# Kernel tuning notes

Measured on AMD Instinct MI355X. Metric: run time of the kernel, lower is better.

The kernel has to match this reference:

```python
import jax, jax.numpy as jnp
import numpy as np

B, L, DIM = 1, 2048, 4096
H, KV, HD = 32, 8, 128
REP = H // KV
SCALE = HD ** -0.5
ROPE_BASE = 10000.0


def rope_traditional(x, offset=0):
    # x: [B, H, L, D] ; traditional RoPE rotates interleaved pairs (x[2i], x[2i+1])
    D = x.shape[-1]
    Lx = x.shape[2]
    pos = jnp.arange(offset, offset + Lx, dtype=jnp.float32)            # [L]
    inv_freq = ROPE_BASE ** (-jnp.arange(0, D, 2, dtype=jnp.float32) / D)  # [D/2]
    ang = pos[:, None] * inv_freq[None, :]                               # [L, D/2]
    c, s = jnp.cos(ang), jnp.sin(ang)
    x1 = x[..., 0::2]
    x2 = x[..., 1::2]
    r1 = x1 * c - x2 * s
    r2 = x1 * s + x2 * c
    return jnp.stack([r1, r2], axis=-1).reshape(x.shape).astype(x.dtype)


def setup_inputs() -> dict:
    key = jax.random.key(0)
    k0, k1, k2, k3, k4 = jax.random.split(key, 5)
    x = jax.random.normal(k0, (B, L, DIM), dtype=jnp.float32)
    wq = jax.random.normal(k1, (DIM, H * HD), dtype=jnp.float32) * 0.02
    wk = jax.random.normal(k2, (DIM, KV * HD), dtype=jnp.float32) * 0.02
    wv = jax.random.normal(k3, (DIM, KV * HD), dtype=jnp.float32) * 0.02
    wo = jax.random.normal(k4, (H * HD, DIM), dtype=jnp.float32) * 0.02
    # additive causal mask (prefill)
    causal = jnp.tril(jnp.ones((L, L), dtype=bool))
    mask = jnp.where(causal, 0.0, -1e9).astype(jnp.float32)
    return {"x": x, "wq": wq, "wk": wk, "wv": wv, "wo": wo, "mask": mask}


def reference(x, wq, wk, wv, wo, mask):
    Bx, Lx, _ = x.shape
    q = (x @ wq).reshape(Bx, Lx, H, HD).transpose(0, 2, 1, 3)   # [B,H,L,hd]
    k = (x @ wk).reshape(Bx, Lx, KV, HD).transpose(0, 2, 1, 3)  # [B,KV,L,hd]
    v = (x @ wv).reshape(Bx, Lx, KV, HD).transpose(0, 2, 1, 3)
    # GQA head repeat (each kv head repeated REP times contiguously)
    k = jnp.repeat(k, REP, axis=1)  # [B,H,L,hd]
    v = jnp.repeat(v, REP, axis=1)
    # RoPE applied after repeat (cache=None branch), offset 0
    q = rope_traditional(q)
    k = rope_traditional(k)
    scores = jnp.einsum("bhld,bhmd->bhlm", q * SCALE, k) + mask  # [B,H,L,L]
    probs = jax.nn.softmax(scores.astype(jnp.float32), axis=-1).astype(scores.dtype)
    out = jnp.einsum("bhlm,bhmd->bhld", probs, v)
    out = out.transpose(0, 2, 1, 3).reshape(Bx, Lx, H * HD)
    return out @ wo, k, v
```

## Files before the change

kernel.cpp:

```cpp
#include <hip/hip_runtime.h>
#include <hip/hip_bf16.h>
#include <math.h>


#define L_SEQ 2048
#define DIM   4096
#define NH    32
#define NKV   8
#define HD    128
#define SCALE 0.08838834764831845f

typedef __bf16 bf16x8 __attribute__((ext_vector_type(8)));
typedef __bf16 bf16x4 __attribute__((ext_vector_type(4)));
typedef __bf16 bf16x2 __attribute__((ext_vector_type(2)));
typedef float  f32x4  __attribute__((ext_vector_type(4)));

__device__ __forceinline__ void gld16(const void* g, void* l) {
  __builtin_amdgcn_global_load_lds(
      (const __attribute__((address_space(1))) void*)g,
      (__attribute__((address_space(3))) void*)l, 16, 0, 0);
}

__global__ void cast_bf16_kernel(const float* __restrict__ in,
                                 __bf16* __restrict__ out, long n4) {
  long i = blockIdx.x * (long)blockDim.x + threadIdx.x;
  if (i >= n4) return;
  float4 f = reinterpret_cast<const float4*>(in)[i];
  bf16x4 o;
  o[0] = (__bf16)f.x; o[1] = (__bf16)f.y; o[2] = (__bf16)f.z; o[3] = (__bf16)f.w;
  reinterpret_cast<bf16x4*>(out)[i] = o;
}

__global__ void tcast_kernel(const float* __restrict__ in0, __bf16* __restrict__ out0,
                             const float* __restrict__ in1, __bf16* __restrict__ out1,
                             int K, int N) {
  __shared__ float tile[32][33];
  const float* in  = blockIdx.z ? in1  : in0;
  __bf16*     out  = blockIdx.z ? out1 : out0;
  int n0 = blockIdx.x * 32, k0 = blockIdx.y * 32;
  int tx = threadIdx.x & 31, ty = threadIdx.x >> 5;
#pragma unroll
  for (int i = 0; i < 4; ++i)
    tile[ty + i * 8][tx] = in[(long)(k0 + ty + i * 8) * N + n0 + tx];
  __syncthreads();
#pragma unroll
  for (int i = 0; i < 4; ++i)
    out[(long)(n0 + ty + i * 8) * K + k0 + tx] = (__bf16)tile[tx][ty + i * 8];
}

__global__ __launch_bounds__(256) void gemm128(
    const __bf16* __restrict__ A, const __bf16* __restrict__ B0,
    const __bf16* __restrict__ B1, void* __restrict__ C0, void* __restrict__ C1,
    int M, int N, int K, int mode) {
  __shared__ __bf16 As[128 * 64] __attribute__((aligned(16)));
  __shared__ __bf16 Bs[128 * 64] __attribute__((aligned(16)));
  const __bf16* Bt = blockIdx.z ? B1 : B0;
  void* C = blockIdx.z ? C1 : C0;
  const int m0 = blockIdx.y * 128, n0 = blockIdx.x * 128;
  const int t = threadIdx.x, wave = t >> 6, lane = t & 63;
  const int quad = lane >> 4, l16 = lane & 15;
  const int wm = (wave >> 1) * 64, wn = (wave & 1) * 64;

  int ar[4], ak[4];
#pragma unroll
  for (int it = 0; it < 4; ++it) {
    int c = it * 256 + t;
    ar[it] = c >> 3;
    ak[it] = ((c & 7) ^ (ar[it] & 7)) * 8;
  }

  f32x4 acc[4][4] = {};

  for (int kt = 0; kt < K; kt += 64) {
    __syncthreads();
#pragma unroll
    for (int it = 0; it < 4; ++it) {
      gld16(A  + (long)(m0 + ar[it]) * K + kt + ak[it],
            (char*)As + (size_t)(it * 256 + wave * 64) * 16);
      gld16(Bt + (long)(n0 + ar[it]) * K + kt + ak[it],
            (char*)Bs + (size_t)(it * 256 + wave * 64) * 16);
    }
    __syncthreads();
#pragma unroll
    for (int ks = 0; ks < 2; ++ks) {
      bf16x8 af[4], bfr[4];
      const int sw = ((ks * 4 + quad) ^ (l16 & 7)) * 16;
#pragma unroll
      for (int i = 0; i < 4; ++i) {
        af[i]  = *(const bf16x8*)((char*)As + (wm + i * 16 + l16) * 128 + sw);
        bfr[i] = *(const bf16x8*)((char*)Bs + (wn + i * 16 + l16) * 128 + sw);
      }
#pragma unroll
      for (int tm = 0; tm < 4; ++tm)
#pragma unroll
        for (int tn = 0; tn < 4; ++tn)
          acc[tm][tn] = __builtin_amdgcn_mfma_f32_16x16x32_bf16(
              af[tm], bfr[tn], acc[tm][tn], 0, 0, 0);
    }
  }
#pragma unroll
  for (int tm = 0; tm < 4; ++tm)
#pragma unroll
    for (int tn = 0; tn < 4; ++tn)
#pragma unroll
      for (int r = 0; r < 4; ++r) {
        int row = m0 + wm + tm * 16 + quad * 4 + r;
        int col = n0 + wn + tn * 16 + l16;
        float v = acc[tm][tn][r];
        if (mode == 0) {
          ((float*)C)[(long)row * N + col] = v;
        } else {
          long idx = ((long)(col >> 7) * L_SEQ + row) * HD + (col & 127);
          ((__bf16*)C)[idx] = (__bf16)v;
        }
      }
}

#define NLOG2_10K 13.287712379549449f

__global__ void rope_q_kernel(__bf16* __restrict__ q ) {
  int idx = blockIdx.x * blockDim.x + threadIdx.x;
  int i = idx & 63, l = (idx >> 6) & 2047, h = idx >> 17;
  if (h >= NH) return;
  long base = ((long)h * L_SEQ + l) * HD + 2 * i;
  bf16x2 x12 = *(bf16x2*)(q + base);
  float x1 = (float)x12[0], x2 = (float)x12[1];
  float inv = exp2f((float)i * (-NLOG2_10K / 64.0f));
  float s, c; __sincosf((float)l * inv, &s, &c);
  bf16x2 o; o[0] = (__bf16)(x1 * c - x2 * s); o[1] = (__bf16)(x1 * s + x2 * c);
  *(bf16x2*)(q + base) = o;
}

__global__ void ropekv_kernel(__bf16* __restrict__ kb ,
                              const __bf16* __restrict__ vb,
                              float* __restrict__ kout ,
                              float* __restrict__ vout) {
  int idx = blockIdx.x * blockDim.x + threadIdx.x;
  int i = idx & 63, l = (idx >> 6) & 2047, kv = idx >> 17;
  if (kv >= NKV) return;
  long base = ((long)kv * L_SEQ + l) * HD + 2 * i;
  bf16x2 x12 = *(bf16x2*)(kb + base);
  float x1 = (float)x12[0], x2 = (float)x12[1];
  float inv = exp2f((float)i * (-NLOG2_10K / 64.0f));
  float s, c; __sincosf((float)l * inv, &s, &c);
  float r1 = x1 * c - x2 * s, r2 = x1 * s + x2 * c;
  bf16x2 o; o[0] = (__bf16)r1; o[1] = (__bf16)r2;
  *(bf16x2*)(kb + base) = o;
  float2 kf; kf.x = r1; kf.y = r2;
  bf16x2 vv = *(const bf16x2*)(vb + base);
  float2 vf; vf.x = (float)vv[0]; vf.y = (float)vv[1];
  long off = (long)(kv * 4) * L_SEQ * HD + (long)l * HD + 2 * i;
#pragma unroll
  for (int rr = 0; rr < 4; ++rr) {
    *(float2*)(kout + off) = kf;
    *(float2*)(vout + off) = vf;
    off += (long)L_SEQ * HD;
  }
}

__global__ void vtrans_kernel(const __bf16* __restrict__ Vh, __bf16* __restrict__ Vt) {
  __shared__ __bf16 tile[64 * 65];
  int kv = blockIdx.z, lb = blockIdx.x * 64, db = blockIdx.y * 64;
  int t = threadIdx.x;
#pragma unroll
  for (int it = 0; it < 2; ++it) {
    int c = it * 256 + t, r = c >> 3, pc = c & 7;
    bf16x8 v = *(const bf16x8*)(Vh + ((long)kv * L_SEQ + lb + r) * HD + db + pc * 8);
#pragma unroll
    for (int e = 0; e < 8; ++e) tile[r * 65 + pc * 8 + e] = v[e];
  }
  __syncthreads();
#pragma unroll
  for (int it = 0; it < 2; ++it) {
    int c = it * 256 + t, r = c >> 3, pc = c & 7;
    bf16x8 v;
#pragma unroll
    for (int e = 0; e < 8; ++e) v[e] = tile[(pc * 8 + e) * 65 + r];
    *(bf16x8*)(Vt + ((long)kv * HD + db + r) * L_SEQ + lb + pc * 8) = v;
  }
}

#define PSP 72

__global__ __launch_bounds__(256) void attn3_kernel(
    const __bf16* __restrict__ Q, const __bf16* __restrict__ K,
    const __bf16* __restrict__ Vt, __bf16* __restrict__ O ) {
  __shared__ __bf16 Ks[2][64 * 128]  __attribute__((aligned(16)));
  __shared__ __bf16 Vts[2][128 * 64] __attribute__((aligned(16)));
  __shared__ __bf16 Ps[64 * PSP]     __attribute__((aligned(16)));

  const int p = blockIdx.x;
  const int h = blockIdx.y;
  const int t = threadIdx.x, wave = t >> 6, lane = t & 63;
  const int quad = lane >> 4, l16 = lane & 15;
  const int mw = wave * 16;
  const __bf16* Kh = K  + (long)(h >> 2) * L_SEQ * HD;
  const __bf16* Vh = Vt + (long)(h >> 2) * HD * L_SEQ;
  const float SL2 = SCALE * 1.44269504f;

  int kr[4], kk[4], vr[4], vk[4];
#pragma unroll
  for (int it = 0; it < 4; ++it) {
    int c = it * 256 + t;
    kr[it] = c >> 4; kk[it] = ((c & 15) ^ (kr[it] & 7)) * 8;
    vr[it] = c >> 3; vk[it] = ((c & 7)  ^ (vr[it] & 7)) * 8;
  }

#pragma unroll 1
  for (int tsel = 0; tsel < 2; ++tsel) {
    const int qb = tsel ? (31 - p) : p;
    const int l0 = qb * 64;
    const int mq = l0 + mw + l16;

    bf16x8 bq[4];
    {
      const __bf16* qrow = Q + ((long)h * L_SEQ + mq) * HD + quad * 8;
#pragma unroll
      for (int d = 0; d < 4; ++d) bq[d] = *(const bf16x8*)(qrow + d * 32);
    }

    f32x4 o_acc[8] = {};
    float m_run = -1e30f, l_run = 0.f;

    __syncthreads();
#pragma unroll
    for (int it = 0; it < 4; ++it) {
      gld16(Kh + (long)(0 + kr[it]) * HD + kk[it],
            (char*)Ks[0] + (size_t)(it * 256 + wave * 64) * 16);
      gld16(Vh + (long)vr[it] * L_SEQ + 0 + vk[it],
            (char*)Vts[0] + (size_t)(it * 256 + wave * 64) * 16);
    }

#pragma unroll 1
    for (int j = 0; j <= qb; ++j) {
      const int cur = j & 1;
      __syncthreads();
      if (j < qb) {
        const int nxt = cur ^ 1;
#pragma unroll
        for (int it = 0; it < 4; ++it) {
          gld16(Kh + (long)((j + 1) * 64 + kr[it]) * HD + kk[it],
                (char*)Ks[nxt] + (size_t)(it * 256 + wave * 64) * 16);
          gld16(Vh + (long)vr[it] * L_SEQ + (j + 1) * 64 + vk[it],
                (char*)Vts[nxt] + (size_t)(it * 256 + wave * 64) * 16);
        }
      }

      f32x4 s[4] = {};
#pragma unroll
      for (int dsi = 0; dsi < 4; ++dsi)
#pragma unroll
        for (int tn = 0; tn < 4; ++tn) {
          bf16x8 ak = *(const bf16x8*)((char*)Ks[cur] + (tn * 16 + l16) * 256 +
                                       (((dsi * 4 + quad) ^ (l16 & 7)) * 16));
          s[tn] = __builtin_amdgcn_mfma_f32_16x16x32_bf16(ak, bq[dsi], s[tn], 0, 0, 0);
        }

#pragma unroll
      for (int tn = 0; tn < 4; ++tn)
#pragma unroll
        for (int r = 0; r < 4; ++r) {
          float v = s[tn][r] * SL2;
          if (j == qb && (j * 64 + tn * 16 + quad * 4 + r) > mq) v = -3.0e38f;
          s[tn][r] = v;
        }
      float mx = -3.0e38f;
#pragma unroll
      for (int tn = 0; tn < 4; ++tn)
#pragma unroll
        for (int r = 0; r < 4; ++r) mx = fmaxf(mx, s[tn][r]);
      mx = fmaxf(mx, __shfl_xor(mx, 16, 64));
      mx = fmaxf(mx, __shfl_xor(mx, 32, 64));
      float mnew = fmaxf(m_run, mx);
      float alpha = exp2f(m_run - mnew);
      float rs = 0.f;
#pragma unroll
      for (int tn = 0; tn < 4; ++tn)
#pragma unroll
        for (int r = 0; r < 4; ++r) {
          float pe = exp2f(s[tn][r] - mnew);
          s[tn][r] = pe; rs += pe;
        }
      rs += __shfl_xor(rs, 16, 64);
      rs += __shfl_xor(rs, 32, 64);
      l_run = l_run * alpha + rs;
      m_run = mnew;

#pragma unroll
      for (int tn = 0; tn < 4; ++tn) {
        bf16x4 pv;
#pragma unroll
        for (int r = 0; r < 4; ++r) pv[r] = (__bf16)s[tn][r];
        *(bf16x4*)(&Ps[(mw + l16) * PSP + tn * 16 + quad * 4]) = pv;
      }

#pragma unroll
      for (int td = 0; td < 8; ++td)
#pragma unroll
        for (int r = 0; r < 4; ++r) o_acc[td][r] *= alpha;
#pragma unroll
      for (int ks = 0; ks < 2; ++ks) {
        bf16x8 bp = *(const bf16x8*)(&Ps[(mw + l16) * PSP + ks * 32 + quad * 8]);
#pragma unroll
        for (int td = 0; td < 8; ++td) {
          bf16x8 av = *(const bf16x8*)((char*)Vts[cur] + (td * 16 + l16) * 128 +
                                       (((ks * 4 + quad) ^ (l16 & 7)) * 16));
          o_acc[td] = __builtin_amdgcn_mfma_f32_16x16x32_bf16(av, bp, o_acc[td], 0, 0, 0);
        }
      }
    }

    float inv_l = 1.0f / l_run;
#pragma unroll
    for (int td = 0; td < 8; ++td) {
      bf16x4 ov;
#pragma unroll
      for (int r = 0; r < 4; ++r) ov[r] = (__bf16)(o_acc[td][r] * inv_l);
      *(bf16x4*)(O + (long)mq * DIM + h * HD + td * 16 + quad * 4) = ov;
    }
  }
}

extern "C" void kernel_launch(void* const* d_in, const int* in_sizes, int n_in,
                              void* d_out, int out_size, void* d_ws, size_t ws_size,
                              hipStream_t stream) {
  const float* x  = (const float*)d_in[0];
  const float* wq = (const float*)d_in[1];
  const float* wk = (const float*)d_in[2];
  const float* wv = (const float*)d_in[3];
  const float* wo = (const float*)d_in[4];

  float* out   = (float*)d_out;
  float* k_out = out + (long)L_SEQ * DIM;
  float* v_out = k_out + (long)NH * L_SEQ * HD;

  char* ws = (char*)d_ws;
  __bf16* Xb  = (__bf16*)ws; ws += (long)L_SEQ * DIM * 2;
  __bf16* Wqt = (__bf16*)ws; ws += (long)DIM * DIM * 2;
  __bf16* Wkt = (__bf16*)ws; ws += (long)DIM * (NKV * HD) * 2;
  __bf16* Wvt = (__bf16*)ws; ws += (long)DIM * (NKV * HD) * 2;
  __bf16* Wot = (__bf16*)ws; ws += (long)DIM * DIM * 2;
  __bf16* Qh  = (__bf16*)ws; ws += (long)NH * L_SEQ * HD * 2;
  __bf16* Kh  = (__bf16*)ws; ws += (long)NKV * L_SEQ * HD * 2;
  __bf16* Vh  = (__bf16*)ws; ws += (long)NKV * L_SEQ * HD * 2;
  __bf16* Vt  = (__bf16*)ws; ws += (long)NKV * HD * L_SEQ * 2;
  __bf16* Ob  = (__bf16*)ws; ws += (long)L_SEQ * DIM * 2;

  tcast_kernel<<<dim3(DIM / 32, DIM / 32, 1), 256, 0, stream>>>(wq, Wqt, wq, Wqt, DIM, DIM);
  tcast_kernel<<<dim3((NKV * HD) / 32, DIM / 32, 2), 256, 0, stream>>>(wk, Wkt, wv, Wvt, DIM, NKV * HD);
  tcast_kernel<<<dim3(DIM / 32, DIM / 32, 1), 256, 0, stream>>>(wo, Wot, wo, Wot, DIM, DIM);
  {
    long n = (long)L_SEQ * DIM;
    cast_bf16_kernel<<<dim3(n / 1024), 256, 0, stream>>>(x, Xb, n / 4);
  }
  gemm128<<<dim3(DIM / 128, L_SEQ / 128, 1), 256, 0, stream>>>(
      Xb, Wqt, Wqt, Qh, Qh, L_SEQ, DIM, DIM, 2);
  gemm128<<<dim3((NKV * HD) / 128, L_SEQ / 128, 2), 256, 0, stream>>>(
      Xb, Wkt, Wvt, Kh, Vh, L_SEQ, NKV * HD, DIM, 2);
  rope_q_kernel<<<dim3((NH * L_SEQ * 64) / 256), 256, 0, stream>>>(Qh);
  ropekv_kernel<<<dim3((NKV * L_SEQ * 64) / 256), 256, 0, stream>>>(Kh, Vh, k_out, v_out);
  vtrans_kernel<<<dim3(L_SEQ / 64, HD / 64, NKV), 256, 0, stream>>>(Vh, Vt);
  attn3_kernel<<<dim3(16, NH), 256, 0, stream>>>(Qh, Kh, Vt, Ob);
  gemm128<<<dim3(DIM / 128, L_SEQ / 128, 1), 256, 0, stream>>>(
      Ob, Wot, Wot, out, out, L_SEQ, DIM, DIM, 0);
}
```

Before: 615.1 us.

## Replace 128x128 GEMM with triple-buffered 128x256 pipelined GEMM and block swizzle

The projection GEMM moves from 128x128 tiles on 256 threads to 128x256 tiles on 512 threads. It uses a three-stage LDS ring filled by async global-to-LDS loads, and `s_waitcnt vmcnt` lets the next tile's loads overlap the current tile's MFMAs instead of forcing a full sync every K step. A workgroup index swizzle is meant to improve L2 reuse, and `s_setprio` raises priority around the MFMA bursts. The cost is about 144KB of LDS per block, so occupancy is limited to one block per CU, and the KV projection now launches fewer workgroups.

```diff
diff --git a/kernel.cpp b/kernel.cpp
--- a/kernel.cpp
+++ b/kernel.cpp
@@ -48,56 +48,136 @@
     out[(long)(n0 + ty + i * 8) * K + k0 + tx] = (__bf16)tile[tx][ty + i * 8];
 }
 
-__global__ __launch_bounds__(256) void gemm128(
+#define GBM 128
+#define GBN 256
+#define ABYTES  (GBM * 64 * 2)
+#define BBYTES  (GBN * 64 * 2)
+#define BUFBYTES (ABYTES + BBYTES)
+
+__global__ __launch_bounds__(512, 2) void gemm256(
     const __bf16* __restrict__ A, const __bf16* __restrict__ B0,
     const __bf16* __restrict__ B1, void* __restrict__ C0, void* __restrict__ C1,
     int M, int N, int K, int mode) {
-  __shared__ __bf16 As[128 * 64] __attribute__((aligned(16)));
-  __shared__ __bf16 Bs[128 * 64] __attribute__((aligned(16)));
+  __shared__ char lds[3 * BUFBYTES] __attribute__((aligned(16)));
   const __bf16* Bt = blockIdx.z ? B1 : B0;
   void* C = blockIdx.z ? C1 : C0;
-  const int m0 = blockIdx.y * 128, n0 = blockIdx.x * 128;
+
+  const int nwg = gridDim.x * gridDim.y;
+  const int bid = blockIdx.y * gridDim.x + blockIdx.x;
+  const int swz = (bid & 7) * (nwg >> 3) + (bid >> 3);
+  const int n0 = (swz % gridDim.x) * GBN;
+  const int m0 = (swz / gridDim.x) * GBM;
+
   const int t = threadIdx.x, wave = t >> 6, lane = t & 63;
   const int quad = lane >> 4, l16 = lane & 15;
-  const int wm = (wave >> 1) * 64, wn = (wave & 1) * 64;
-
-  int ar[4], ak[4];
-#pragma unroll
-  for (int it = 0; it < 4; ++it) {
-    int c = it * 256 + t;
-    ar[it] = c >> 3;
-    ak[it] = ((c & 7) ^ (ar[it] & 7)) * 8;
+  const int wm = (wave >> 2) * 64, wn = (wave & 3) * 64;
+
+  const int srow = t >> 3;
+  const int scol = ((t & 7) ^ (srow & 7)) * 8;
+  const __bf16* pa = A  + (long)(m0 + srow) * K + scol;
+  const __bf16* pb = Bt + (long)(n0 + srow) * K + scol;
+  const long K64 = (long)64 * K;
+  const int ldsA = wave * 1024;
+  const int ldsB = ABYTES + wave * 1024;
+
+  int aoff[2][4], boff[2][4];
+#pragma unroll
+  for (int ks = 0; ks < 2; ++ks) {
+    const int sw = ((ks * 4 + quad) ^ (l16 & 7)) * 16;
+#pragma unroll
+    for (int i = 0; i < 4; ++i) {
+      aoff[ks][i] = (wm + i * 16 + l16) * 128 + sw;
+      boff[ks][i] = ABYTES + (wn + i * 16 + l16) * 128 + sw;
+    }
   }
 
   f32x4 acc[4][4] = {};
-
-  for (int kt = 0; kt < K; kt += 64) {
-    __syncthreads();
-#pragma unroll
-    for (int it = 0; it < 4; ++it) {
-      gld16(A  + (long)(m0 + ar[it]) * K + kt + ak[it],
-            (char*)As + (size_t)(it * 256 + wave * 64) * 16);
-      gld16(Bt + (long)(n0 + ar[it]) * K + kt + ak[it],
-            (char*)Bs + (size_t)(it * 256 + wave * 64) * 16);
-    }
-    __syncthreads();
+  const int nt = K >> 6;
+
+  {
+    char* bb = lds;
+#pragma unroll
+    for (int pt = 0; pt < 2; ++pt) {
+      gld16(pa,           bb + ldsA);
+      gld16(pa + K64,     bb + ldsA + 8192);
+      gld16(pb,           bb + ldsB);
+      gld16(pb + K64,     bb + ldsB + 8192);
+      gld16(pb + 2 * K64, bb + ldsB + 16384);
+      gld16(pb + 3 * K64, bb + ldsB + 24576);
+      pa += 64; pb += 64;
+      bb += BUFBYTES;
+    }
+  }
+
+  char* cb = lds;
+  char* sb = lds + 2 * BUFBYTES;
+
+#pragma unroll 1
+  for (int kt = 0; kt < nt - 1; ++kt) {
+    asm volatile("s_waitcnt vmcnt(6)" ::: "memory");
+    __builtin_amdgcn_s_barrier();
+    bf16x8 af[4], bfr[4];
+#pragma unroll
+    for (int i = 0; i < 4; ++i) {
+      af[i]  = *(const bf16x8*)(cb + aoff[0][i]);
+      bfr[i] = *(const bf16x8*)(cb + boff[0][i]);
+    }
+    if (kt + 2 < nt) {
+      gld16(pa,           sb + ldsA);
+      gld16(pa + K64,     sb + ldsA + 8192);
+      gld16(pb,           sb + ldsB);
+      gld16(pb + K64,     sb + ldsB + 8192);
+      gld16(pb + 2 * K64, sb + ldsB + 16384);
+      gld16(pb + 3 * K64, sb + ldsB + 24576);
+      pa += 64; pb += 64;
+    }
+    __builtin_amdgcn_s_setprio(1);
+#pragma unroll
+    for (int tm = 0; tm < 4; ++tm)
+#pragma unroll
+      for (int tn = 0; tn < 4; ++tn)
+        acc[tm][tn] = __builtin_amdgcn_mfma_f32_16x16x32_bf16(
+            af[tm], bfr[tn], acc[tm][tn], 0, 0, 0);
+    __builtin_amdgcn_s_setprio(0);
+#pragma unroll
+    for (int i = 0; i < 4; ++i) {
+      af[i]  = *(const bf16x8*)(cb + aoff[1][i]);
+      bfr[i] = *(const bf16x8*)(cb + boff[1][i]);
+    }
+    __builtin_amdgcn_s_setprio(1);
+#pragma unroll
+    for (int tm = 0; tm < 4; ++tm)
+#pragma unroll
+      for (int tn = 0; tn < 4; ++tn)
+        acc[tm][tn] = __builtin_amdgcn_mfma_f32_16x16x32_bf16(
+            af[tm], bfr[tn], acc[tm][tn], 0, 0, 0);
+    __builtin_amdgcn_s_setprio(0);
+    cb += BUFBYTES; if (cb == lds + 3 * BUFBYTES) cb = lds;
+    sb += BUFBYTES; if (sb == lds + 3 * BUFBYTES) sb = lds;
+  }
+
+  asm volatile("s_waitcnt vmcnt(0)" ::: "memory");
+  __builtin_amdgcn_s_barrier();
+  {
+    bf16x8 af[4], bfr[4];
 #pragma unroll
     for (int ks = 0; ks < 2; ++ks) {
-      bf16x8 af[4], bfr[4];
-      const int sw = ((ks * 4 + quad) ^ (l16 & 7)) * 16;
 #pragma unroll
       for (int i = 0; i < 4; ++i) {
-        af[i]  = *(const bf16x8*)((char*)As + (wm + i * 16 + l16) * 128 + sw);
-        bfr[i] = *(const bf16x8*)((char*)Bs + (wn + i * 16 + l16) * 128 + sw);
+        af[i]  = *(const bf16x8*)(cb + aoff[ks][i]);
+        bfr[i] = *(const bf16x8*)(cb + boff[ks][i]);
       }
+      __builtin_amdgcn_s_setprio(1);
 #pragma unroll
       for (int tm = 0; tm < 4; ++tm)
 #pragma unroll
         for (int tn = 0; tn < 4; ++tn)
           acc[tm][tn] = __builtin_amdgcn_mfma_f32_16x16x32_bf16(
               af[tm], bfr[tn], acc[tm][tn], 0, 0, 0);
-    }
-  }
+      __builtin_amdgcn_s_setprio(0);
+    }
+  }
+
 #pragma unroll
   for (int tm = 0; tm < 4; ++tm)
 #pragma unroll
@@ -353,14 +433,14 @@
     long n = (long)L_SEQ * DIM;
     cast_bf16_kernel<<<dim3(n / 1024), 256, 0, stream>>>(x, Xb, n / 4);
   }
-  gemm128<<<dim3(DIM / 128, L_SEQ / 128, 1), 256, 0, stream>>>(
+  gemm256<<<dim3(DIM / 256, L_SEQ / 128, 1), 512, 0, stream>>>(
       Xb, Wqt, Wqt, Qh, Qh, L_SEQ, DIM, DIM, 2);
-  gemm128<<<dim3((NKV * HD) / 128, L_SEQ / 128, 2), 256, 0, stream>>>(
+  gemm256<<<dim3((NKV * HD) / 256, L_SEQ / 128, 2), 512, 0, stream>>>(
       Xb, Wkt, Wvt, Kh, Vh, L_SEQ, NKV * HD, DIM, 2);
   rope_q_kernel<<<dim3((NH * L_SEQ * 64) / 256), 256, 0, stream>>>(Qh);
   ropekv_kernel<<<dim3((NKV * L_SEQ * 64) / 256), 256, 0, stream>>>(Kh, Vh, k_out, v_out);
   vtrans_kernel<<<dim3(L_SEQ / 64, HD / 64, NKV), 256, 0, stream>>>(Vh, Vt);
   attn3_kernel<<<dim3(16, NH), 256, 0, stream>>>(Qh, Kh, Vt, Ob);
-  gemm128<<<dim3(DIM / 128, L_SEQ / 128, 1), 256, 0, stream>>>(
+  gemm256<<<dim3(DIM / 256, L_SEQ / 128, 1), 512, 0, stream>>>(
       Ob, Wot, Wot, out, out, L_SEQ, DIM, DIM, 0);
 }
```

Result: faster. 550.1 us (-10.6%).
